# Optimization experiments

Measured on AMD Instinct MI355X. Metric: run time of the kernel, lower is better.

Reference implementation:

```python
import jax, jax.numpy as jnp
import numpy as np

N, J, P = 512, 20000, 8   # samples, genes (rna_count), covariates
DIM = J - 1               # pivot=True drops one column from the softmax logits


def setup_inputs() -> dict:
    key = jax.random.key(0)
    k0, k1, k2, k3, k4 = jax.random.split(key, 5)
    X = jax.random.normal(k0, (N, P), dtype=jnp.float32)
    # counts: non-negative integers stored as float (matches torch float64 Y of counts)
    Y = jnp.round(jax.random.uniform(k1, (N, J), dtype=jnp.float32) * 1000.0)
    mu = jax.random.normal(k2, (DIM,), dtype=jnp.float32)
    beta = jax.random.normal(k3, (P * DIM,), dtype=jnp.float32) * 0.1
    phi = jax.random.normal(k4, (J,), dtype=jnp.float32)
    return {"mu": mu, "beta": beta, "phi": phi, "X": X, "Y": Y}


def _nb_loglik(y, mean, disp):
    # NB with mean `mean` and dispersion `disp` (var = mean + disp*mean^2):
    # r = 1/disp, p = r/(r+mean)
    # log pmf = lgamma(y+r) - lgamma(r) - lgamma(y+1) + r*log(p) + y*log(1-p)
    r = 1.0 / disp
    log_rpm = jnp.log(r + mean)
    return (jax.lax.lgamma(y + r) - jax.lax.lgamma(r) - jax.lax.lgamma(y + 1.0)
            + r * (jnp.log(r) - log_rpm)
            + y * (jnp.log(mean) - log_rpm))


def reference(mu, beta, phi, X, Y):
    n, p = X.shape
    dim = mu.shape[0]
    beta_ = beta.reshape(p, dim)
    logits = mu + X @ beta_                                   # [N, J-1]
    logits = jnp.concatenate(
        [logits, jnp.zeros((n, 1), dtype=logits.dtype)], axis=1)  # pivot column of zeros -> [N, J]
    pi = jax.nn.softmax(logits, axis=1)                       # exp(logits - logsumexp)
    s = jnp.sum(Y, axis=1, keepdims=True)                     # [N, 1] total counts per sample
    mean = s * pi                                             # [N, J]
    disp = jax.nn.softplus(phi)                               # [J]
    log_lik = jnp.sum(_nb_loglik(Y, mean, disp))
    return log_lik.reshape(1)
```

## Files before the change

### kernel.cpp

```cpp
#include <hip/hip_runtime.h>
#include <hip/hip_bf16.h>

constexpr int N_SAMPLES = 512;
constexpr int J_GENES   = 20000;
constexpr int P_COV     = 8;
constexpr int DIM       = J_GENES - 1;
constexpr int BLOCK     = 256;
constexpr int CHUNK     = 1024;
constexpr int CPR       = (J_GENES + CHUNK - 1) / CHUNK;
constexpr int TABLE_N   = 1024;

constexpr size_t WS_RW    = 0;
constexpr size_t WS_LOGRW = WS_RW    + J_GENES;
constexpr size_t WS_LGRW  = WS_LOGRW + J_GENES;
constexpr size_t WS_MUP   = WS_LGRW  + J_GENES;
constexpr size_t WS_BETAP = WS_MUP   + J_GENES;
constexpr size_t WS_LGYT  = WS_BETAP + (size_t)P_COV * J_GENES;
constexpr size_t WS_SACC  = WS_LGYT  + TABLE_N;
constexpr size_t WS_EACC  = WS_SACC  + N_SAMPLES;
constexpr size_t WS_PART  = WS_EACC  + N_SAMPLES;
constexpr size_t WS_TOTAL = WS_PART  + (size_t)N_SAMPLES * CPR;

__device__ inline float wave_reduce_sum(float v) {
#pragma unroll
    for (int off = 32; off > 0; off >>= 1)
        v += __shfl_down(v, off, 64);
    return v;
}

__device__ inline float lgamma_pos(float z) {
    float corr = 0.0f;
    if (z < 8.0f) {
        float p = z;
        p *= (z + 1.0f); p *= (z + 2.0f); p *= (z + 3.0f);
        p *= (z + 4.0f); p *= (z + 5.0f); p *= (z + 6.0f); p *= (z + 7.0f);
        corr = -__logf(p);
        z += 8.0f;
    }
    float lz  = __logf(z);
    float rz  = __builtin_amdgcn_rcpf(z);
    float rz2 = rz * rz;
    float ser = rz * fmaf(rz2, fmaf(rz2, 7.9365079365e-4f, -2.7777777778e-3f),
                          8.3333333333e-2f);
    return fmaf(z - 0.5f, lz, 0.91893853320467274f - z + ser + corr);
}

__global__ __launch_bounds__(BLOCK) void prep_kernel(
    const float* __restrict__ mu, const float* __restrict__ beta,
    const float* __restrict__ phi, float* __restrict__ ws) {
    int j = blockIdx.x * blockDim.x + threadIdx.x;
    if (j < N_SAMPLES) { ws[WS_SACC + j] = 0.0f; ws[WS_EACC + j] = 0.0f; }
    if (j < TABLE_N)   ws[WS_LGYT + j] = lgammaf((float)j + 1.0f);
    if (j < J_GENES) {
        float ph = phi[j];
        float sp = (ph > 20.0f) ? ph : log1pf(__expf(ph));
        float r  = 1.0f / sp;
        ws[WS_RW    + j] = r;
        ws[WS_LOGRW + j] = -__logf(sp);
        ws[WS_LGRW  + j] = lgammaf(r);
        ws[WS_MUP   + j] = (j < DIM) ? mu[j] : 0.0f;
#pragma unroll
        for (int p = 0; p < P_COV; ++p)
            ws[WS_BETAP + (size_t)p * J_GENES + j] =
                (j < DIM) ? beta[p * DIM + j] : 0.0f;
    }
}

__global__ __launch_bounds__(BLOCK) void pass1_kernel(
    const float* __restrict__ X, const float* __restrict__ Y,
    const float* __restrict__ ws_c, float* __restrict__ ws) {
    const int n = blockIdx.y;
    const int t = threadIdx.x;
    const int j = blockIdx.x * CHUNK + t * 4;

    float x[P_COV];
#pragma unroll
    for (int p = 0; p < P_COV; ++p) x[p] = X[n * P_COV + p];

    float s_acc = 0.0f, e_acc = 0.0f;
    if (j < J_GENES) {
        float4 y4 = *(const float4*)(Y + (size_t)n * J_GENES + j);
        float4 lg = *(const float4*)(ws_c + WS_MUP + j);
#pragma unroll
        for (int p = 0; p < P_COV; ++p) {
            float4 b = *(const float4*)(ws_c + WS_BETAP + (size_t)p * J_GENES + j);
            lg.x = fmaf(x[p], b.x, lg.x);
            lg.y = fmaf(x[p], b.y, lg.y);
            lg.z = fmaf(x[p], b.z, lg.z);
            lg.w = fmaf(x[p], b.w, lg.w);
        }
        s_acc = (y4.x + y4.y) + (y4.z + y4.w);
        e_acc = (__expf(lg.x) + __expf(lg.y)) + (__expf(lg.z) + __expf(lg.w));
    }

    float vs = wave_reduce_sum(s_acc);
    float ve = wave_reduce_sum(e_acc);
    __shared__ float rs[4], re[4];
    if ((t & 63) == 0) { rs[t >> 6] = vs; re[t >> 6] = ve; }
    __syncthreads();
    if (t == 0) {
        atomicAdd(&ws[WS_SACC + n], (rs[0] + rs[1]) + (rs[2] + rs[3]));
        atomicAdd(&ws[WS_EACC + n], (re[0] + re[1]) + (re[2] + re[3]));
    }
}

__device__ inline float nb_term(float y, float logit, float r, float logr,
                                float lgr, float s, float logs, float lse,
                                const float* __restrict__ tbl) {
    float lp   = logit - lse;
    float mean = s * __expf(lp);
    float lrm  = __logf(r + mean);
    int   yi   = (int)(y + 0.5f);
    float lgy1 = (yi >= 0 && yi < TABLE_N) ? tbl[yi] : lgamma_pos(y + 1.0f);
    float lgyr = lgamma_pos(y + r);
    return lgyr - lgr - lgy1 + fmaf(r, logr - lrm, y * ((logs + lp) - lrm));
}

__global__ __launch_bounds__(BLOCK) void pass2_kernel(
    const float* __restrict__ X, const float* __restrict__ Y,
    const float* __restrict__ ws_c, float* __restrict__ ws) {
    const int n = blockIdx.y;
    const int t = threadIdx.x;
    const int j = blockIdx.x * CHUNK + t * 4;

    __shared__ __align__(16) float tbl[TABLE_N];
    __shared__ float shv[3];
    *(float4*)&tbl[t * 4] = *(const float4*)(ws_c + WS_LGYT + t * 4);
    if (t == 0) {
        float s = ws_c[WS_SACC + n];
        float E = ws_c[WS_EACC + n];
        shv[0] = s; shv[1] = __logf(s); shv[2] = __logf(E);
    }
    __syncthreads();
    const float s = shv[0], logs = shv[1], lse = shv[2];

    float x[P_COV];
#pragma unroll
    for (int p = 0; p < P_COV; ++p) x[p] = X[n * P_COV + p];

    float acc = 0.0f;
    if (j < J_GENES) {
        float4 y4  = *(const float4*)(Y + (size_t)n * J_GENES + j);
        float4 lg  = *(const float4*)(ws_c + WS_MUP + j);
#pragma unroll
        for (int p = 0; p < P_COV; ++p) {
            float4 b = *(const float4*)(ws_c + WS_BETAP + (size_t)p * J_GENES + j);
            lg.x = fmaf(x[p], b.x, lg.x);
            lg.y = fmaf(x[p], b.y, lg.y);
            lg.z = fmaf(x[p], b.z, lg.z);
            lg.w = fmaf(x[p], b.w, lg.w);
        }
        float4 r4  = *(const float4*)(ws_c + WS_RW    + j);
        float4 lr4 = *(const float4*)(ws_c + WS_LOGRW + j);
        float4 lg4 = *(const float4*)(ws_c + WS_LGRW  + j);
        acc  = nb_term(y4.x, lg.x, r4.x, lr4.x, lg4.x, s, logs, lse, tbl);
        acc += nb_term(y4.y, lg.y, r4.y, lr4.y, lg4.y, s, logs, lse, tbl);
        acc += nb_term(y4.z, lg.z, r4.z, lr4.z, lg4.z, s, logs, lse, tbl);
        acc += nb_term(y4.w, lg.w, r4.w, lr4.w, lg4.w, s, logs, lse, tbl);
    }

    float v = wave_reduce_sum(acc);
    __shared__ float red[4];
    if ((t & 63) == 0) red[t >> 6] = v;
    __syncthreads();
    if (t == 0)
        ws[WS_PART + (size_t)n * CPR + blockIdx.x] =
            (red[0] + red[1]) + (red[2] + red[3]);
}

__global__ __launch_bounds__(BLOCK) void final_kernel(
    const float* __restrict__ ws_c, float* __restrict__ out) {
    const int t = threadIdx.x;
    float acc = 0.0f;
    for (int i = t; i < N_SAMPLES * CPR; i += BLOCK)
        acc += ws_c[WS_PART + i];
    float v = wave_reduce_sum(acc);
    __shared__ float red[4];
    if ((t & 63) == 0) red[t >> 6] = v;
    __syncthreads();
    if (t == 0) out[0] = (red[0] + red[1]) + (red[2] + red[3]);
}

__global__ __launch_bounds__(BLOCK) void nb_mono(
    const float* __restrict__ mu, const float* __restrict__ beta,
    const float* __restrict__ phi, const float* __restrict__ X,
    const float* __restrict__ Y, float* __restrict__ out) {
    const int n = blockIdx.x;
    const int t = threadIdx.x;
    __shared__ float red[4];
    __shared__ float sh_s, sh_lse, sh_logs;
    float x[P_COV];
#pragma unroll
    for (int p = 0; p < P_COV; ++p) x[p] = X[n * P_COV + p];
    const float* yrow = Y + (size_t)n * J_GENES;
    float s_acc = 0.0f, e_acc = 0.0f;
    for (int j = t; j < J_GENES; j += BLOCK) {
        float logit = 0.0f;
        if (j < DIM) {
            logit = mu[j];
#pragma unroll
            for (int p = 0; p < P_COV; ++p)
                logit = fmaf(x[p], beta[p * DIM + j], logit);
        }
        s_acc += yrow[j];
        e_acc += __expf(logit);
    }
    float v = wave_reduce_sum(s_acc);
    if ((t & 63) == 0) red[t >> 6] = v;
    __syncthreads();
    if (t == 0) { float st = red[0]+red[1]+red[2]+red[3]; sh_s = st; sh_logs = __logf(st); }
    __syncthreads();
    v = wave_reduce_sum(e_acc);
    if ((t & 63) == 0) red[t >> 6] = v;
    __syncthreads();
    if (t == 0) sh_lse = __logf(red[0]+red[1]+red[2]+red[3]);
    __syncthreads();
    const float s = sh_s, logs = sh_logs, lse = sh_lse;
    float acc = 0.0f;
    for (int j = t; j < J_GENES; j += BLOCK) {
        float logit = 0.0f;
        if (j < DIM) {
            logit = mu[j];
#pragma unroll
            for (int p = 0; p < P_COV; ++p)
                logit = fmaf(x[p], beta[p * DIM + j], logit);
        }
        float ph = phi[j];
        float sp = (ph > 20.0f) ? ph : log1pf(__expf(ph));
        float r  = 1.0f / sp;
        float y  = yrow[j];
        float lp = logit - lse;
        float mean = s * __expf(lp);
        float lrm  = __logf(r + mean);
        acc += lgamma_pos(y + r) - lgamma_pos(r) - lgamma_pos(y + 1.0f)
             + fmaf(r, -__logf(sp) - lrm, y * ((logs + lp) - lrm));
    }
    v = wave_reduce_sum(acc);
    if ((t & 63) == 0) red[t >> 6] = v;
    __syncthreads();
    if (t == 0) atomicAdd(out, (red[0]+red[1])+(red[2]+red[3]));
}

__global__ void zero_out_kernel(float* __restrict__ out) { out[0] = 0.0f; }

extern "C" void kernel_launch(void* const* d_in, const int* in_sizes, int n_in,
                              void* d_out, int out_size, void* d_ws, size_t ws_size,
                              hipStream_t stream) {
    const float* mu   = (const float*)d_in[0];
    const float* beta = (const float*)d_in[1];
    const float* phi  = (const float*)d_in[2];
    const float* X    = (const float*)d_in[3];
    const float* Y    = (const float*)d_in[4];
    float* out = (float*)d_out;
    float* ws  = (float*)d_ws;

    if (ws_size >= WS_TOTAL * sizeof(float)) {
        dim3 grid(CPR, N_SAMPLES);
        prep_kernel<<<(J_GENES + BLOCK - 1) / BLOCK, BLOCK, 0, stream>>>(
            mu, beta, phi, ws);
        pass1_kernel<<<grid, BLOCK, 0, stream>>>(X, Y, ws, ws);
        pass2_kernel<<<grid, BLOCK, 0, stream>>>(X, Y, ws, ws);
        final_kernel<<<1, BLOCK, 0, stream>>>(ws, out);
    } else {
        zero_out_kernel<<<1, 1, 0, stream>>>(out);
        nb_mono<<<N_SAMPLES, BLOCK, 0, stream>>>(mu, beta, phi, X, Y, out);
    }
}
```

Baseline: 150.7 us.

## Fuse softmax-sum and NB loglik passes into one per-sample register-resident kernel

Replaces the pass1/pass2/final kernels with a single kernel where one 1024-thread block handles one sample row. Y and exp(logits) are held in registers between the normalizer reduction and the log-likelihood pass, so Y is read once and the logits are not recomputed. The final reduction now uses atomics. The lgamma shift is also cut from 8 to 2 steps and mean is computed as (s/E)*exp(logit). Risks include higher register pressure with 5 float4 pairs per thread, only 512 blocks, reduced lgamma accuracy for small arguments, and nondeterministic atomic summation.

```diff
diff --git a/kernel.cpp b/kernel.cpp
--- a/kernel.cpp
+++ b/kernel.cpp
@@ -6,8 +6,9 @@
 constexpr int P_COV     = 8;
 constexpr int DIM       = J_GENES - 1;
 constexpr int BLOCK     = 256;
-constexpr int CHUNK     = 1024;
-constexpr int CPR       = (J_GENES + CHUNK - 1) / CHUNK;
+constexpr int TPB       = 1024;
+constexpr int SWEEP_G   = TPB * 4;
+constexpr int SWEEPS    = (J_GENES + SWEEP_G - 1) / SWEEP_G;
 constexpr int TABLE_N   = 1024;
 
 constexpr size_t WS_RW    = 0;
@@ -16,10 +17,7 @@
 constexpr size_t WS_MUP   = WS_LGRW  + J_GENES;
 constexpr size_t WS_BETAP = WS_MUP   + J_GENES;
 constexpr size_t WS_LGYT  = WS_BETAP + (size_t)P_COV * J_GENES;
-constexpr size_t WS_SACC  = WS_LGYT  + TABLE_N;
-constexpr size_t WS_EACC  = WS_SACC  + N_SAMPLES;
-constexpr size_t WS_PART  = WS_EACC  + N_SAMPLES;
-constexpr size_t WS_TOTAL = WS_PART  + (size_t)N_SAMPLES * CPR;
+constexpr size_t WS_TOTAL = WS_LGYT  + TABLE_N;
 
 __device__ inline float wave_reduce_sum(float v) {
 #pragma unroll
@@ -30,12 +28,9 @@
 
 __device__ inline float lgamma_pos(float z) {
     float corr = 0.0f;
-    if (z < 8.0f) {
-        float p = z;
-        p *= (z + 1.0f); p *= (z + 2.0f); p *= (z + 3.0f);
-        p *= (z + 4.0f); p *= (z + 5.0f); p *= (z + 6.0f); p *= (z + 7.0f);
-        corr = -__logf(p);
-        z += 8.0f;
+    if (z < 2.0f) {
+        corr = -__logf(z * (z + 1.0f));
+        z += 2.0f;
     }
     float lz  = __logf(z);
     float rz  = __builtin_amdgcn_rcpf(z);
@@ -47,10 +42,11 @@
 
 __global__ __launch_bounds__(BLOCK) void prep_kernel(
     const float* __restrict__ mu, const float* __restrict__ beta,
-    const float* __restrict__ phi, float* __restrict__ ws) {
+    const float* __restrict__ phi, float* __restrict__ ws,
+    float* __restrict__ out) {
     int j = blockIdx.x * blockDim.x + threadIdx.x;
-    if (j < N_SAMPLES) { ws[WS_SACC + j] = 0.0f; ws[WS_EACC + j] = 0.0f; }
-    if (j < TABLE_N)   ws[WS_LGYT + j] = lgammaf((float)j + 1.0f);
+    if (j == 0) out[0] = 0.0f;
+    if (j < TABLE_N) ws[WS_LGYT + j] = lgammaf((float)j + 1.0f);
     if (j < J_GENES) {
         float ph = phi[j];
         float sp = (ph > 20.0f) ? ph : log1pf(__expf(ph));
@@ -66,119 +62,101 @@
     }
 }
 
-__global__ __launch_bounds__(BLOCK) void pass1_kernel(
+__device__ inline float nb_term(float y, float el, float r, float logr,
+                                float lgr, float c,
+                                const float* __restrict__ tbl) {
+    float mean = c * el;
+    float lm   = __logf(mean);
+    float lrm  = __logf(r + mean);
+    int   yi   = (int)(y + 0.5f);
+    float lgy1 = (yi < TABLE_N) ? tbl[yi] : lgamma_pos(y + 1.0f);
+    float lgyr = lgamma_pos(y + r);
+    return lgyr - lgr - lgy1 + fmaf(r, logr - lrm, y * (lm - lrm));
+}
+
+__global__ __launch_bounds__(TPB) void fused_kernel(
     const float* __restrict__ X, const float* __restrict__ Y,
-    const float* __restrict__ ws_c, float* __restrict__ ws) {
-    const int n = blockIdx.y;
+    const float* __restrict__ ws_c, float* __restrict__ out) {
+    const int n = blockIdx.x;
     const int t = threadIdx.x;
-    const int j = blockIdx.x * CHUNK + t * 4;
+
+    __shared__ __align__(16) float tbl[TABLE_N];
+    __shared__ float rs[TPB / 64], re[TPB / 64];
+    __shared__ float sh_c;
+
+    tbl[t] = ws_c[WS_LGYT + t];
 
     float x[P_COV];
 #pragma unroll
     for (int p = 0; p < P_COV; ++p) x[p] = X[n * P_COV + p];
 
+    const float* __restrict__ yrow = Y + (size_t)n * J_GENES;
+
+    float4 y4[SWEEPS], e4[SWEEPS];
     float s_acc = 0.0f, e_acc = 0.0f;
-    if (j < J_GENES) {
-        float4 y4 = *(const float4*)(Y + (size_t)n * J_GENES + j);
-        float4 lg = *(const float4*)(ws_c + WS_MUP + j);
-#pragma unroll
-        for (int p = 0; p < P_COV; ++p) {
-            float4 b = *(const float4*)(ws_c + WS_BETAP + (size_t)p * J_GENES + j);
-            lg.x = fmaf(x[p], b.x, lg.x);
-            lg.y = fmaf(x[p], b.y, lg.y);
-            lg.z = fmaf(x[p], b.z, lg.z);
-            lg.w = fmaf(x[p], b.w, lg.w);
-        }
-        s_acc = (y4.x + y4.y) + (y4.z + y4.w);
-        e_acc = (__expf(lg.x) + __expf(lg.y)) + (__expf(lg.z) + __expf(lg.w));
+#pragma unroll
+    for (int w = 0; w < SWEEPS; ++w) {
+        const int j = w * SWEEP_G + t * 4;
+        if (j < J_GENES) {
+            float4 yy = *(const float4*)(yrow + j);
+            float4 lg = *(const float4*)(ws_c + WS_MUP + j);
+#pragma unroll
+            for (int p = 0; p < P_COV; ++p) {
+                float4 b = *(const float4*)(ws_c + WS_BETAP + (size_t)p * J_GENES + j);
+                lg.x = fmaf(x[p], b.x, lg.x);
+                lg.y = fmaf(x[p], b.y, lg.y);
+                lg.z = fmaf(x[p], b.z, lg.z);
+                lg.w = fmaf(x[p], b.w, lg.w);
+            }
+            float4 ee = make_float4(__expf(lg.x), __expf(lg.y),
+                                    __expf(lg.z), __expf(lg.w));
+            y4[w] = yy;
+            e4[w] = ee;
+            s_acc += (yy.x + yy.y) + (yy.z + yy.w);
+            e_acc += (ee.x + ee.y) + (ee.z + ee.w);
+        } else {
+            y4[w] = make_float4(0.f, 0.f, 0.f, 0.f);
+            e4[w] = make_float4(0.f, 0.f, 0.f, 0.f);
+        }
     }
 
     float vs = wave_reduce_sum(s_acc);
     float ve = wave_reduce_sum(e_acc);
-    __shared__ float rs[4], re[4];
     if ((t & 63) == 0) { rs[t >> 6] = vs; re[t >> 6] = ve; }
     __syncthreads();
     if (t == 0) {
-        atomicAdd(&ws[WS_SACC + n], (rs[0] + rs[1]) + (rs[2] + rs[3]));
-        atomicAdd(&ws[WS_EACC + n], (re[0] + re[1]) + (re[2] + re[3]));
-    }
-}
-
-__device__ inline float nb_term(float y, float logit, float r, float logr,
-                                float lgr, float s, float logs, float lse,
-                                const float* __restrict__ tbl) {
-    float lp   = logit - lse;
-    float mean = s * __expf(lp);
-    float lrm  = __logf(r + mean);
-    int   yi   = (int)(y + 0.5f);
-    float lgy1 = (yi >= 0 && yi < TABLE_N) ? tbl[yi] : lgamma_pos(y + 1.0f);
-    float lgyr = lgamma_pos(y + r);
-    return lgyr - lgr - lgy1 + fmaf(r, logr - lrm, y * ((logs + lp) - lrm));
-}
-
-__global__ __launch_bounds__(BLOCK) void pass2_kernel(
-    const float* __restrict__ X, const float* __restrict__ Y,
-    const float* __restrict__ ws_c, float* __restrict__ ws) {
-    const int n = blockIdx.y;
-    const int t = threadIdx.x;
-    const int j = blockIdx.x * CHUNK + t * 4;
-
-    __shared__ __align__(16) float tbl[TABLE_N];
-    __shared__ float shv[3];
-    *(float4*)&tbl[t * 4] = *(const float4*)(ws_c + WS_LGYT + t * 4);
+        float s = 0.0f, E = 0.0f;
+#pragma unroll
+        for (int i = 0; i < TPB / 64; ++i) { s += rs[i]; E += re[i]; }
+        sh_c = s / E;
+    }
+    __syncthreads();
+    const float c = sh_c;
+
+    float acc = 0.0f;
+#pragma unroll
+    for (int w = 0; w < SWEEPS; ++w) {
+        const int j = w * SWEEP_G + t * 4;
+        if (j < J_GENES) {
+            float4 r4  = *(const float4*)(ws_c + WS_RW    + j);
+            float4 lr4 = *(const float4*)(ws_c + WS_LOGRW + j);
+            float4 lg4 = *(const float4*)(ws_c + WS_LGRW  + j);
+            acc += nb_term(y4[w].x, e4[w].x, r4.x, lr4.x, lg4.x, c, tbl);
+            acc += nb_term(y4[w].y, e4[w].y, r4.y, lr4.y, lg4.y, c, tbl);
+            acc += nb_term(y4[w].z, e4[w].z, r4.z, lr4.z, lg4.z, c, tbl);
+            acc += nb_term(y4[w].w, e4[w].w, r4.w, lr4.w, lg4.w, c, tbl);
+        }
+    }
+
+    float v = wave_reduce_sum(acc);
+    if ((t & 63) == 0) rs[t >> 6] = v;
+    __syncthreads();
     if (t == 0) {
-        float s = ws_c[WS_SACC + n];
-        float E = ws_c[WS_EACC + n];
-        shv[0] = s; shv[1] = __logf(s); shv[2] = __logf(E);
-    }
-    __syncthreads();
-    const float s = shv[0], logs = shv[1], lse = shv[2];
-
-    float x[P_COV];
-#pragma unroll
-    for (int p = 0; p < P_COV; ++p) x[p] = X[n * P_COV + p];
-
-    float acc = 0.0f;
-    if (j < J_GENES) {
-        float4 y4  = *(const float4*)(Y + (size_t)n * J_GENES + j);
-        float4 lg  = *(const float4*)(ws_c + WS_MUP + j);
-#pragma unroll
-        for (int p = 0; p < P_COV; ++p) {
-            float4 b = *(const float4*)(ws_c + WS_BETAP + (size_t)p * J_GENES + j);
-            lg.x = fmaf(x[p], b.x, lg.x);
-            lg.y = fmaf(x[p], b.y, lg.y);
-            lg.z = fmaf(x[p], b.z, lg.z);
-            lg.w = fmaf(x[p], b.w, lg.w);
-        }
-        float4 r4  = *(const float4*)(ws_c + WS_RW    + j);
-        float4 lr4 = *(const float4*)(ws_c + WS_LOGRW + j);
-        float4 lg4 = *(const float4*)(ws_c + WS_LGRW  + j);
-        acc  = nb_term(y4.x, lg.x, r4.x, lr4.x, lg4.x, s, logs, lse, tbl);
-        acc += nb_term(y4.y, lg.y, r4.y, lr4.y, lg4.y, s, logs, lse, tbl);
-        acc += nb_term(y4.z, lg.z, r4.z, lr4.z, lg4.z, s, logs, lse, tbl);
-        acc += nb_term(y4.w, lg.w, r4.w, lr4.w, lg4.w, s, logs, lse, tbl);
-    }
-
-    float v = wave_reduce_sum(acc);
-    __shared__ float red[4];
-    if ((t & 63) == 0) red[t >> 6] = v;
-    __syncthreads();
-    if (t == 0)
-        ws[WS_PART + (size_t)n * CPR + blockIdx.x] =
-            (red[0] + red[1]) + (red[2] + red[3]);
-}
-
-__global__ __launch_bounds__(BLOCK) void final_kernel(
-    const float* __restrict__ ws_c, float* __restrict__ out) {
-    const int t = threadIdx.x;
-    float acc = 0.0f;
-    for (int i = t; i < N_SAMPLES * CPR; i += BLOCK)
-        acc += ws_c[WS_PART + i];
-    float v = wave_reduce_sum(acc);
-    __shared__ float red[4];
-    if ((t & 63) == 0) red[t >> 6] = v;
-    __syncthreads();
-    if (t == 0) out[0] = (red[0] + red[1]) + (red[2] + red[3]);
+        float tot = 0.0f;
+#pragma unroll
+        for (int i = 0; i < TPB / 64; ++i) tot += rs[i];
+        atomicAdd(out, tot);
+    }
 }
 
 __global__ __launch_bounds__(BLOCK) void nb_mono(
@@ -255,12 +233,9 @@
     float* ws  = (float*)d_ws;
 
     if (ws_size >= WS_TOTAL * sizeof(float)) {
-        dim3 grid(CPR, N_SAMPLES);
         prep_kernel<<<(J_GENES + BLOCK - 1) / BLOCK, BLOCK, 0, stream>>>(
-            mu, beta, phi, ws);
-        pass1_kernel<<<grid, BLOCK, 0, stream>>>(X, Y, ws, ws);
-        pass2_kernel<<<grid, BLOCK, 0, stream>>>(X, Y, ws, ws);
-        final_kernel<<<1, BLOCK, 0, stream>>>(ws, out);
+            mu, beta, phi, ws, out);
+        fused_kernel<<<N_SAMPLES, TPB, 0, stream>>>(X, Y, ws, out);
     } else {
         zero_out_kernel<<<1, 1, 0, stream>>>(out);
         nb_mono<<<N_SAMPLES, BLOCK, 0, stream>>>(mu, beta, phi, X, Y, out);
```

Measured after the change: 126.3 us. 16.2% less time.
